# Optimization experiments

Hardware: AMD Instinct MI355X
Metric: run time of the kernel (lower is better)

The kernel has to match this reference:

```python
import jax, jax.numpy as jnp
import numpy as np

CURVE = 1.0
TAU = 0.5
N_NODES = 32768
N_EDGES = 65536
IN_CH = 64
OUT_CH = 64
N_HEADS = 8
N_RF = 128
EPS = 1e-7


def _make_projection_matrix(m, d, seed=0):
    # FAVOR+ projection: stacked rows of transposed QR blocks, row-rescaled by chi norms.
    rng = np.random.RandomState(seed)
    blocks = []
    nb_full = m // d
    for _ in range(nb_full):
        q, _ = np.linalg.qr(rng.randn(d, d))
        blocks.append(q.T)
    rem = m - nb_full * d
    if rem > 0:
        q, _ = np.linalg.qr(rng.randn(d, d))
        blocks.append(q.T[:rem])
    final = np.vstack(blocks)  # [m, d]
    mult = np.linalg.norm(rng.randn(m, d), axis=1)
    return (mult[:, None] * final).astype(np.float32)


def _expmap0(u, c):
    # Hyperboloid exp map at origin; time slot of u is ignored.
    sqrtK = 1.0 / jnp.sqrt(c)
    x = u[..., 1:]
    xn = jnp.maximum(jnp.linalg.norm(x, axis=-1, keepdims=True), EPS)
    theta = xn / sqrtK
    return jnp.concatenate([sqrtK * jnp.cosh(theta), sqrtK * jnp.sinh(theta) * x / xn], axis=-1)


def _proj(x, c):
    # Re-project onto hyperboloid: x0 = sqrt(1/c + ||x_space||^2)
    K = 1.0 / c
    y = x[..., 1:]
    t = jnp.sqrt(K + jnp.sum(y * y, axis=-1, keepdims=True))
    return jnp.concatenate([t, y], axis=-1)


def _logmap0(x, c):
    # Hyperboloid log map at origin; output tangent has zero time component.
    sqrtK = 1.0 / jnp.sqrt(c)
    y = x[..., 1:]
    yn = jnp.maximum(jnp.linalg.norm(y, axis=-1, keepdims=True), EPS)
    t = jnp.maximum(x[..., 0:1] / sqrtK, 1.0 + EPS)
    res = sqrtK * jnp.arccosh(t) * y / yn
    return jnp.concatenate([jnp.zeros_like(res[..., :1]), res], axis=-1)


def _softmax_kernel(data, P, tau, c):
    # Performer-style exp kernel with hyperbolic (time-coordinate) prefactor.
    dt = data[..., 0:1]
    ds = data[..., 1:]
    m = 1.0 / jnp.sqrt(jnp.asarray(P.shape[0], jnp.float32))
    wx = jnp.exp(jnp.einsum('bnhd,dm->bnhm', ds, P) / jnp.sqrt(tau))
    front = jnp.exp((c / tau - dt * dt / tau) / 2.0) * m  # [b,n,h,1]
    return wx * front


def setup_inputs() -> dict:
    key = jax.random.key(0)
    k1, k2, k3, k4 = jax.random.split(key, 4)
    std = (2.0 / (IN_CH + OUT_CH)) ** 0.5
    z = 0.01 * jax.random.normal(k1, (1, N_NODES, IN_CH), jnp.float32)
    Wq = std * jax.random.normal(k2, (N_HEADS, OUT_CH, IN_CH), jnp.float32)
    Wk = std * jax.random.normal(k3, (N_HEADS, OUT_CH, IN_CH), jnp.float32)
    Wv = std * jax.random.normal(k4, (N_HEADS, OUT_CH, IN_CH), jnp.float32)
    edge_index = jax.random.randint(jax.random.fold_in(key, 7), (2, N_EDGES), 0, N_NODES, jnp.int32)
    proj_mat = jnp.asarray(_make_projection_matrix(IN_CH - 1, N_RF))  # [63, 128]
    return {"z": z, "Wq": Wq, "Wk": Wk, "Wv": Wv, "proj_mat": proj_mat, "edge_index": edge_index}


def reference(z, Wq, Wk, Wv, proj_mat, edge_index):
    c = jnp.float32(CURVE)
    tau = jnp.float32(TAU)
    zs = z[0]  # [N, C] (B == 1, squeeze)
    zh = _proj(_expmap0(zs, c), c)  # lift features to hyperboloid
    u = _logmap0(zh, c)             # [N, C], tangent at origin

    def hyplin(W):  # HypLinear (no bias): proj(expmap0(logmap0(x) @ W^T)) for all heads
        mu = jnp.einsum('nc,hoc->hno', u, W)  # [H, N, D]
        return _proj(_expmap0(mu, c), c)

    q, k, v = hyplin(Wq), hyplin(Wk), hyplin(Wv)  # [H, N, D]
    H, N, D = q.shape
    # mirrors torch stacked.reshape(-1, N, H, D) (row-major relabeling)
    query = q.reshape(1, N, H, D)
    key_ = k.reshape(1, N, H, D)
    value = v.reshape(1, N, H, D)

    qp = _softmax_kernel(query, proj_mat, tau, c).transpose(2, 0, 1, 3)  # [H,1,N,M]
    kp = _softmax_kernel(key_, proj_mat, tau, c).transpose(2, 0, 1, 3)   # [H,1,N,M]
    vv = value.transpose(2, 0, 1, 3)                                      # [H,1,N,D]

    last = jnp.einsum('hbnm,hbnd->hbmd', kp, vv)   # [H,1,M,D] kv summary
    zo = jnp.einsum('hbnm,hbmd->hbnd', qp, last)   # [H,1,N,D]
    mnorm = -zo[..., 0:1] ** 2 + jnp.sum(zo[..., 1:] ** 2, axis=-1, keepdims=True)
    zo = zo / (jnp.sqrt(c) * jnp.sqrt(jnp.abs(mnorm)))  # renormalize onto hyperboloid

    start, end = edge_index[0], edge_index[1]
    ea = jnp.einsum('hbem,hbem->hbe', qp[:, :, end, :], kp[:, :, start, :])
    A_weight = ea.transpose(1, 2, 0)  # [1, E, H]

    # hyper_agg: Euclidean head-mean followed by Minkowski renormalization
    t = jnp.mean(zo[:, 0], axis=0)  # [N, D]
    xn = -t[..., 0:1] ** 2 + jnp.sum(t[..., 1:] ** 2, axis=-1, keepdims=True)
    z_next = t / (jnp.sqrt(c) * jnp.sqrt(jnp.abs(xn)))
    link_loss = jnp.mean(A_weight)
    return z_next, link_loss
```

## Files before the change

### kernel.cpp

```cpp
#include <hip/hip_runtime.h>

#define DEV __device__ __forceinline__

#define NNODES 32768
#define NEDGES 65536
#define NROWS  262144
#define EPSF   1e-7f
#define SQRT2F 1.4142135623730951f
#define LOG2E  1.4426950408889634f
#define LOG2SQRT63 2.9886399611087573f

#define OFF_WFRAG 0u
#define OFF_LASTB 0u
#define OFF_PFRAG 196608u
#define OFF_EA    212992u
#define OFF_U     409600u
#define OFF_PART  42352640u
#define OFF_PHIQ  75907072u
#define OFF_PHIK  143015936u

typedef short s8v __attribute__((ext_vector_type(8)));
typedef float f4v __attribute__((ext_vector_type(4)));
typedef float f2v __attribute__((ext_vector_type(2)));

DEV unsigned short f2bf(float f) {
  unsigned u = __float_as_uint(f);
  return (unsigned short)((u + 0x7fffu + ((u >> 16) & 1u)) >> 16);
}
DEV float bf2f(unsigned short h) { return __uint_as_float(((unsigned)h) << 16); }
DEV unsigned pack2(float lo, float hi) {
  return __builtin_amdgcn_perm(__float_as_uint(hi) + 0x8000u, __float_as_uint(lo) + 0x8000u, 0x07060302u);
}
DEV float frcp(float x) { return __builtin_amdgcn_rcpf(x); }
DEV float fsqrt(float x) { return __builtin_amdgcn_sqrtf(x); }
DEV float fexp2(float x) { return __builtin_amdgcn_exp2f(x); }

__global__ __launch_bounds__(256) void k01_prep(const float* __restrict__ z, unsigned short* __restrict__ ubf,
                                                const float* __restrict__ Wq, const float* __restrict__ Wk,
                                                const float* __restrict__ Wv, const float* __restrict__ P,
                                                unsigned short* __restrict__ Wfrag, unsigned short* __restrict__ Pfrag,
                                                float* __restrict__ ea) {
  int i = blockIdx.x * 256 + threadIdx.x;
  float4 v = *(const float4*)(z + (size_t)i * 4);
  if ((i & 15) == 0) v.x = 0.f;
  uint2 pk;
  pk.x = pack2(v.x, v.y);
  pk.y = pack2(v.z, v.w);
  *(uint2*)(ubf + (size_t)i * 4) = pk;

  if (blockIdx.x < 96) {
    if (i == 0) ea[0] = 0.f;
    int stride = 96 * 256;
    for (int t = i; t < 98304; t += stride) {
      int j = t & 7, lane = (t >> 3) & 63, nt = (t >> 9) & 3, ks = (t >> 11) & 1, h = (t >> 12) & 7, sm = t >> 15;
      int k = ks * 32 + (lane >> 4) * 8 + j;
      int n = nt * 16 + (lane & 15);
      const float* W = (sm == 0) ? Wq : ((sm == 1) ? Wk : Wv);
      Wfrag[t] = f2bf(W[(h * 64 + n) * 64 + k]);
    }
    for (int t = i; t < 8192; t += stride) {
      int j = t & 7, lane = (t >> 3) & 63, ks = (t >> 9) & 1, mt = (t >> 10) & 7;
      int k = ks * 32 + (lane >> 4) * 8 + j;
      int r = lane & 15;
      int m = ((mt >> 2) << 6) + ((r >> 2) << 4) + ((mt & 3) << 2) + (r & 3);
      Pfrag[t] = (k == 0) ? (unsigned short)0 : f2bf(P[(k - 1) * 128 + m] * (SQRT2F * LOG2E));
    }
  }
}

__global__ __launch_bounds__(256, 4) void k2_mfma(const unsigned short* __restrict__ ubf,
                                                  const unsigned short* __restrict__ Wfrag,
                                                  const unsigned short* __restrict__ Pfrag,
                                                  unsigned char* __restrict__ phiq, unsigned char* __restrict__ phik,
                                                  unsigned char* __restrict__ part8) {
  __shared__ short lds_raw[9472];
  short* sbuf = lds_raw;
  float* sfront = (float*)(lds_raw + 9216);
  unsigned char* kbufT8 = (unsigned char*)lds_raw;
  unsigned char* vbufT8 = (unsigned char*)lds_raw + 9216;

  int w = threadIdx.x >> 6, lane = threadIdx.x & 63;
  int q = lane >> 4, l = lane & 15;
  int b = blockIdx.x;
  int h = b >> 8, t = b & 255;
  int n0 = t * 128 + w * 32;

  s8v afr[2][2];
#pragma unroll
  for (int mt = 0; mt < 2; ++mt)
#pragma unroll
    for (int ks = 0; ks < 2; ++ks)
      afr[mt][ks] = *(const s8v*)(ubf + (size_t)(n0 + mt * 16 + l) * 64 + ks * 32 + q * 8);

  const s8v* Wf = (const s8v*)Wfrag;
  const s8v* Pf = (const s8v*)Pfrag;
  unsigned vk[2][4];
  unsigned keepA[8], keepB[8];

#pragma unroll
  for (int sm = 0; sm < 3; ++sm) {
    f4v acc[2][4];
#pragma unroll
    for (int mt = 0; mt < 2; ++mt)
#pragma unroll
      for (int nt = 0; nt < 4; ++nt) acc[mt][nt] = (f4v)(0.f);
#pragma unroll
    for (int ks = 0; ks < 2; ++ks)
#pragma unroll
      for (int nt = 0; nt < 4; ++nt) {
        s8v bf = Wf[(((sm * 8 + h) * 2 + ks) * 4 + nt) * 64 + lane];
#pragma unroll
        for (int mt = 0; mt < 2; ++mt)
          acc[mt][nt] = __builtin_amdgcn_mfma_f32_16x16x32_bf16(afr[mt][ks], bf, acc[mt][nt], 0, 0, 0);
      }
#pragma unroll
    for (int mt = 0; mt < 2; ++mt) {
      float rs[4];
#pragma unroll
      for (int reg = 0; reg < 4; ++reg) {
        float v0 = (l == 0) ? 0.f : acc[mt][0][reg];
        rs[reg] = v0 * v0 + acc[mt][1][reg] * acc[mt][1][reg] + acc[mt][2][reg] * acc[mt][2][reg] +
                  acc[mt][3][reg] * acc[mt][3][reg];
      }
#pragma unroll
      for (int reg = 0; reg < 4; ++reg) {
#pragma unroll
        for (int off = 1; off < 16; off <<= 1) rs[reg] += __shfl_xor(rs[reg], off, 64);
      }
      float vreg[4][4];
#pragma unroll
      for (int reg = 0; reg < 4; ++reg) {
        float x = fmaxf(fsqrt(rs[reg]), EPSF);
        float e = fexp2(x * LOG2E);
        float sh = 0.5f * (e - frcp(e));
        float ratio = sh * frcp(x);
        float sh2 = sh * sh;
        int row = mt * 16 + q * 4 + reg;
        if (sm == 2) {
          float tt2 = fsqrt(1.f + sh2);
#pragma unroll
          for (int nt = 0; nt < 4; ++nt) {
            float val = acc[mt][nt][reg] * ratio;
            if (l == 0 && nt == 0) val = tt2;
            vreg[nt][reg] = val;
          }
        } else {
          float lf = -sh2 * LOG2E - LOG2SQRT63;
          if (l == 0) sfront[w * 32 + row] = lf;
#pragma unroll
          for (int nt = 0; nt < 4; ++nt) {
            float val = acc[mt][nt][reg] * ratio;
            if (l == 0 && nt == 0) val = 0.f;
            sbuf[w * 2304 + row * 72 + ((nt * 16 + l) ^ ((q >> 1) << 4))] =
                (short)(__float_as_uint(val) >> 16);
          }
        }
      }
      if (sm == 2) {
#pragma unroll
        for (int nt = 0; nt < 4; ++nt) {
          unsigned pv = __builtin_amdgcn_cvt_pk_fp8_f32(vreg[nt][0], vreg[nt][1], 0, 0);
          vk[mt][nt] = __builtin_amdgcn_cvt_pk_fp8_f32(vreg[nt][2], vreg[nt][3], pv, 1);
        }
      }
    }

    if (sm < 2) {
      int fr = (l >> 3) & 1;
      s8v bsf[2][2];
#pragma unroll
      for (int nt = 0; nt < 2; ++nt)
#pragma unroll
        for (int ks = 0; ks < 2; ++ks)
          bsf[nt][ks] = *(const s8v*)&sbuf[w * 2304 + (nt * 16 + l) * 72 + ((ks * 32 + q * 8) ^ (fr << 4))];
      float lf0 = sfront[w * 32 + l];
      float lf1 = sfront[w * 32 + 16 + l];
      unsigned char* dst = sm ? phik : phiq;
      unsigned g0a[4], g0b[4], g1a[4], g1b[4];
#pragma unroll
      for (int mt = 0; mt < 8; ++mt) {
        f4v a0 = (f4v)(0.f), a1 = (f4v)(0.f);
#pragma unroll
        for (int ks = 0; ks < 2; ++ks) {
          s8v ap = Pf[(mt * 2 + ks) * 64 + lane];
          a0 = __builtin_amdgcn_mfma_f32_16x16x32_bf16(ap, bsf[0][ks], a0, 0, 0, 0);
          a1 = __builtin_amdgcn_mfma_f32_16x16x32_bf16(ap, bsf[1][ks], a1, 0, 0, 0);
        }
        float v00 = fexp2(a0[0] + lf0), v01 = fexp2(a0[1] + lf0), v02 = fexp2(a0[2] + lf0), v03 = fexp2(a0[3] + lf0);
        float v10 = fexp2(a1[0] + lf1), v11 = fexp2(a1[1] + lf1), v12 = fexp2(a1[2] + lf1), v13 = fexp2(a1[3] + lf1);
        unsigned p0 = __builtin_amdgcn_cvt_pk_fp8_f32(v00, v01, 0, 0);
        p0 = __builtin_amdgcn_cvt_pk_fp8_f32(v02, v03, p0, 1);
        unsigned p1 = __builtin_amdgcn_cvt_pk_fp8_f32(v10, v11, 0, 0);
        p1 = __builtin_amdgcn_cvt_pk_fp8_f32(v12, v13, p1, 1);
        if (mt < 4) { g0a[mt] = p0; g1a[mt] = p1; }
        else        { g0b[mt - 4] = p0; g1b[mt - 4] = p1; }
        if (sm == 1) { keepA[mt] = p0; keepB[mt] = p1; }
      }
      size_t b0 = (size_t)(n0 + l) * 1024 + (size_t)(h * 128 + q * 16);
      *(uint4*)(dst + b0)              = make_uint4(g0a[0], g0a[1], g0a[2], g0a[3]);
      *(uint4*)(dst + b0 + 64)         = make_uint4(g0b[0], g0b[1], g0b[2], g0b[3]);
      *(uint4*)(dst + b0 + 16384)      = make_uint4(g1a[0], g1a[1], g1a[2], g1a[3]);
      *(uint4*)(dst + b0 + 16384 + 64) = make_uint4(g1b[0], g1b[1], g1b[2], g1b[3]);
    }
  }

  f4v facc[2][4];
#pragma unroll
  for (int mtl = 0; mtl < 2; ++mtl)
#pragma unroll
    for (int nt = 0; nt < 4; ++nt) facc[mtl][nt] = (f4v)(0.f);

#pragma unroll
  for (int hf = 0; hf < 2; ++hf) {
    __syncthreads();
    if ((w >> 1) == hf) {
      int nd0 = (w & 1) * 32 + l, nd1 = nd0 + 16;
      int c0 = nd0 ^ (q << 4), c1 = nd1 ^ (q << 4);
#pragma unroll
      for (int mt = 0; mt < 8; ++mt) {
        int M0 = ((mt >> 2) << 6) + (q << 4) + ((mt & 3) << 2);
        unsigned a = keepA[mt], bq = keepB[mt];
#pragma unroll
        for (int r = 0; r < 4; ++r) {
          kbufT8[(M0 + r) * 72 + c0] = (unsigned char)(a >> (8 * r));
          kbufT8[(M0 + r) * 72 + c1] = (unsigned char)(bq >> (8 * r));
        }
      }
#pragma unroll
      for (int mt = 0; mt < 2; ++mt)
#pragma unroll
        for (int nt = 0; nt < 4; ++nt)
          *(unsigned*)&vbufT8[(nt * 16 + l) * 72 + (w & 1) * 32 + mt * 16 + q * 4] = vk[mt][nt];
    }
    __syncthreads();
#pragma unroll
    for (int kc = 0; kc < 2; ++kc) {
      long bv[4];
#pragma unroll
      for (int nt = 0; nt < 4; ++nt)
        bv[nt] = *(const long*)&vbufT8[(nt * 16 + l) * 72 + kc * 32 + q * 8];
      long av[2];
#pragma unroll
      for (int mtl = 0; mtl < 2; ++mtl) {
        int row = (2 * w + mtl) * 16 + l;
        int cb = (kc * 32 + q * 8) ^ (((2 * w + mtl) & 3) << 4);
        av[mtl] = *(const long*)&kbufT8[row * 72 + cb];
      }
#pragma unroll
      for (int mtl = 0; mtl < 2; ++mtl)
#pragma unroll
        for (int nt = 0; nt < 4; ++nt)
          facc[mtl][nt] = __builtin_amdgcn_mfma_f32_16x16x32_fp8_fp8(av[mtl], bv[nt], facc[mtl][nt], 0, 0, 0);
    }
  }

#pragma unroll
  for (int mtl = 0; mtl < 2; ++mtl)
#pragma unroll
    for (int nt = 0; nt < 4; ++nt) {
      unsigned pk8 = __builtin_amdgcn_cvt_pk_bf8_f32(facc[mtl][nt][0], facc[mtl][nt][1], 0, 0);
      pk8 = __builtin_amdgcn_cvt_pk_bf8_f32(facc[mtl][nt][2], facc[mtl][nt][3], pk8, 1);
      int d = nt * 16 + l;
      int m = (2 * w + mtl) * 16 + q * 4;
      *(unsigned*)(part8 + ((size_t)((t * 8 + h) * 64 + d)) * 128 + m) = pk8;
    }
}

__global__ __launch_bounds__(256) void k35(const unsigned* __restrict__ part32, unsigned char* __restrict__ lastB,
                                           const unsigned char* __restrict__ phiq,
                                           const unsigned char* __restrict__ phik,
                                           const int* __restrict__ ei, float* __restrict__ ea) {
  int b = blockIdx.x;
  if (b < 64) {
    int t2 = b * 256 + threadIdx.x;
    float s0 = 0.f, s1 = 0.f, s2 = 0.f, s3 = 0.f;
#pragma unroll 8
    for (int c = 0; c < 256; ++c) {
      unsigned v = part32[(c << 14) + t2];
      f2v lo = __builtin_amdgcn_cvt_pk_f32_bf8(v, 0);
      f2v hi = __builtin_amdgcn_cvt_pk_f32_bf8(v, 1);
      s0 += lo.x; s1 += lo.y; s2 += hi.x; s3 += hi.y;
    }
    int mq = t2 & 31, d = (t2 >> 5) & 63, h = t2 >> 11;
    int m0 = mq * 4;
    int ks = m0 >> 5, j0 = m0 & 7, qq = (m0 >> 3) & 3;
    int lane = qq * 16 + (d & 15), nt = d >> 4;
    unsigned r = __builtin_amdgcn_cvt_pk_bf8_f32(s0, s1, 0, 0);
    r = __builtin_amdgcn_cvt_pk_bf8_f32(s2, s3, r, 1);
    *(unsigned*)(lastB + ((((h * 4 + ks) * 4 + nt) * 64 + lane) << 3) + j0) = r;
    return;
  }
  __shared__ float part[4];
  int lane = threadIdx.x & 63, w = threadIdx.x >> 6;
  int wid = (b - 64) * 4 + w;
  float acc0 = 0.f, acc1 = 0.f;
#pragma unroll
  for (int i = 0; i < 8; i += 2) {
    int e0 = wid * 8 + i, e1 = e0 + 1;
    int s0 = ei[e0], d0 = ei[NEDGES + e0];
    int s1 = ei[e1], d1 = ei[NEDGES + e1];
    uint4 qa = *(const uint4*)(phiq + (size_t)d0 * 1024 + lane * 16);
    uint4 ka = *(const uint4*)(phik + (size_t)s0 * 1024 + lane * 16);
    uint4 qb = *(const uint4*)(phiq + (size_t)d1 * 1024 + lane * 16);
    uint4 kb = *(const uint4*)(phik + (size_t)s1 * 1024 + lane * 16);
    unsigned qs[8] = {qa.x, qa.y, qa.z, qa.w, qb.x, qb.y, qb.z, qb.w};
    unsigned ks[8] = {ka.x, ka.y, ka.z, ka.w, kb.x, kb.y, kb.z, kb.w};
#pragma unroll
    for (int p = 0; p < 8; ++p) {
      f2v q0 = __builtin_amdgcn_cvt_pk_f32_fp8(qs[p], 0);
      f2v q1 = __builtin_amdgcn_cvt_pk_f32_fp8(qs[p], 1);
      f2v k0 = __builtin_amdgcn_cvt_pk_f32_fp8(ks[p], 0);
      f2v k1 = __builtin_amdgcn_cvt_pk_f32_fp8(ks[p], 1);
      float t0 = fmaf(q0.x, k0.x, q0.y * k0.y);
      float t1 = fmaf(q1.x, k1.x, q1.y * k1.y);
      if (p < 4) acc0 += t0 + t1; else acc1 += t0 + t1;
    }
  }
  float acc = acc0 + acc1;
#pragma unroll
  for (int o = 1; o < 64; o <<= 1) acc += __shfl_xor(acc, o, 64);
  if (lane == 0) part[w] = acc;
  __syncthreads();
  if (threadIdx.x == 0) atomicAdd(ea, part[0] + part[1] + part[2] + part[3]);
}

__global__ __launch_bounds__(512) void k4_mfma(const unsigned char* __restrict__ phiq,
                                               const unsigned char* __restrict__ lastB,
                                               const float* __restrict__ ea, float* __restrict__ out) {
  __shared__ unsigned zbufT[8][64][18];
  int w = threadIdx.x >> 6, lane = threadIdx.x & 63;
  int q = lane >> 4, l = lane & 15;
  int n0 = blockIdx.x * 32;

  const long* Bf = (const long*)lastB;
  long bf[4][4];
#pragma unroll
  for (int ks = 0; ks < 4; ++ks)
#pragma unroll
    for (int nt = 0; nt < 4; ++nt) bf[ks][nt] = Bf[((w * 4 + ks) * 4 + nt) * 64 + lane];

  long af[2][4];
#pragma unroll
  for (int mt = 0; mt < 2; ++mt)
#pragma unroll
    for (int ks = 0; ks < 4; ++ks)
      af[mt][ks] = *(const long*)(phiq + (size_t)(8 * (n0 + mt * 16 + l) + w) * 128 + ks * 32 + q * 8);

  f4v acc[2][4];
#pragma unroll
  for (int mt = 0; mt < 2; ++mt)
#pragma unroll
    for (int nt = 0; nt < 4; ++nt) acc[mt][nt] = (f4v)(0.f);
#pragma unroll
  for (int ks = 0; ks < 4; ++ks)
#pragma unroll
    for (int nt = 0; nt < 4; ++nt)
#pragma unroll
      for (int mt = 0; mt < 2; ++mt)
        acc[mt][nt] = __builtin_amdgcn_mfma_f32_16x16x32_fp8_bf8(af[mt][ks], bf[ks][nt], acc[mt][nt], 0, 0, 0);

#pragma unroll
  for (int mt = 0; mt < 2; ++mt) {
    float rs[4];
#pragma unroll
    for (int reg = 0; reg < 4; ++reg) {
      float v0 = acc[mt][0][reg];
      float s0 = (l == 0) ? -v0 * v0 : v0 * v0;
      rs[reg] = s0 + acc[mt][1][reg] * acc[mt][1][reg] + acc[mt][2][reg] * acc[mt][2][reg] +
                acc[mt][3][reg] * acc[mt][3][reg];
    }
#pragma unroll
    for (int reg = 0; reg < 4; ++reg) {
#pragma unroll
      for (int off = 1; off < 16; off <<= 1) rs[reg] += __shfl_xor(rs[reg], off, 64);
    }
    float inv[4];
#pragma unroll
    for (int reg = 0; reg < 4; ++reg) inv[reg] = frcp(fsqrt(fabsf(rs[reg])));
#pragma unroll
    for (int nt = 0; nt < 4; ++nt) {
      uint2 pk;
      pk.x = pack2(acc[mt][nt][0] * inv[0], acc[mt][nt][1] * inv[1]);
      pk.y = pack2(acc[mt][nt][2] * inv[2], acc[mt][nt][3] * inv[3]);
      *(uint2*)&zbufT[w][nt * 16 + l][mt * 8 + q * 2] = pk;
    }
  }
  __syncthreads();

  int tid = threadIdx.x;
  int i = tid >> 4, dg = tid & 15;
  int i2 = i >> 1, sel = i & 1;
  float s[4] = {0.f, 0.f, 0.f, 0.f};
#pragma unroll
  for (int w2 = 0; w2 < 8; ++w2) {
#pragma unroll
    for (int j = 0; j < 4; ++j) {
      unsigned u = zbufT[w2][dg * 4 + j][i2];
      s[j] += bf2f((unsigned short)(sel ? (u >> 16) : (u & 0xffffu)));
    }
  }
  float m2 = 0.f;
#pragma unroll
  for (int j = 0; j < 4; ++j) {
    s[j] *= 0.125f;
    m2 += ((dg == 0 && j == 0) ? -s[j] * s[j] : s[j] * s[j]);
  }
#pragma unroll
  for (int off = 1; off < 16; off <<= 1) m2 += __shfl_xor(m2, off, 64);
  float inv = frcp(fsqrt(fabsf(m2)));
  float4 o = make_float4(s[0] * inv, s[1] * inv, s[2] * inv, s[3] * inv);
  *(float4*)(out + (size_t)(n0 + i) * 64 + dg * 4) = o;
  if (blockIdx.x == 0 && tid == 0) out[(size_t)NNODES * 64] = ea[0] * (1.0f / 524288.0f);
}

extern "C" void kernel_launch(void* const* d_in, const int* in_sizes, int n_in,
                              void* d_out, int out_size, void* d_ws, size_t ws_size,
                              hipStream_t stream) {
  const float* z  = (const float*)d_in[0];
  const float* Wq = (const float*)d_in[1];
  const float* Wk = (const float*)d_in[2];
  const float* Wv = (const float*)d_in[3];
  const float* P  = (const float*)d_in[4];
  const int* ei   = (const int*)d_in[5];
  char* ws = (char*)d_ws;
  unsigned short* Wfrag = (unsigned short*)(ws + OFF_WFRAG);
  unsigned char*  lastB = (unsigned char*)(ws + OFF_LASTB);
  unsigned short* Pfrag = (unsigned short*)(ws + OFF_PFRAG);
  float*          ea    = (float*)(ws + OFF_EA);
  unsigned short* ubf   = (unsigned short*)(ws + OFF_U);
  unsigned char*  part8 = (unsigned char*)(ws + OFF_PART);
  unsigned char*  phiq  = (unsigned char*)(ws + OFF_PHIQ);
  unsigned char*  phik  = (unsigned char*)(ws + OFF_PHIK);

  k01_prep<<<2048, 256, 0, stream>>>(z, ubf, Wq, Wk, Wv, P, Wfrag, Pfrag, ea);
  k2_mfma<<<2048, 256, 0, stream>>>(ubf, Wfrag, Pfrag, phiq, phik, part8);
  k35<<<64 + 2048, 256, 0, stream>>>((const unsigned*)part8, lastB, phiq, phik, ei, ea);
  k4_mfma<<<NNODES / 32, 512, 0, stream>>>(phiq, lastB, ea, (float*)d_out);
}
```

Baseline: 178.0 us.

## Stage full K/V fp8 tile in LDS directly and raise k2 occupancy

K and V fp8 fragments are now written straight into a larger LDS tile as they are produced, instead of being held in registers and staged in two halves with extra barriers. The KV-summary MFMA loop then runs once over all 128 rows after a single sync, and launch bounds go from 4 to 5 blocks per CU. The aim is to free the keepA/keepB/vk registers and cut barrier count so occupancy can rise. The cost is more LDS per block, which could limit residency, and byte-granular LDS stores now sit inside the phi computation loop.

```diff
diff --git a/kernel.cpp b/kernel.cpp
--- a/kernel.cpp
+++ b/kernel.cpp
@@ -68,16 +68,16 @@
   }
 }
 
-__global__ __launch_bounds__(256, 4) void k2_mfma(const unsigned short* __restrict__ ubf,
+__global__ __launch_bounds__(256, 5) void k2_mfma(const unsigned short* __restrict__ ubf,
                                                   const unsigned short* __restrict__ Wfrag,
                                                   const unsigned short* __restrict__ Pfrag,
                                                   unsigned char* __restrict__ phiq, unsigned char* __restrict__ phik,
                                                   unsigned char* __restrict__ part8) {
-  __shared__ short lds_raw[9472];
+  __shared__ short lds_raw[13312];
   short* sbuf = lds_raw;
-  float* sfront = (float*)(lds_raw + 9216);
-  unsigned char* kbufT8 = (unsigned char*)lds_raw;
-  unsigned char* vbufT8 = (unsigned char*)lds_raw + 9216;
+  float* sfront = (float*)(lds_raw + 13056);
+  unsigned char* kbuf2 = (unsigned char*)lds_raw;
+  unsigned char* vbuf2 = (unsigned char*)lds_raw + 17408;
 
   int w = threadIdx.x >> 6, lane = threadIdx.x & 63;
   int q = lane >> 4, l = lane & 15;
@@ -94,8 +94,6 @@
 
   const s8v* Wf = (const s8v*)Wfrag;
   const s8v* Pf = (const s8v*)Pfrag;
-  unsigned vk[2][4];
-  unsigned keepA[8], keepB[8];
 
 #pragma unroll
   for (int sm = 0; sm < 3; ++sm) {
@@ -160,7 +158,8 @@
 #pragma unroll
         for (int nt = 0; nt < 4; ++nt) {
           unsigned pv = __builtin_amdgcn_cvt_pk_fp8_f32(vreg[nt][0], vreg[nt][1], 0, 0);
-          vk[mt][nt] = __builtin_amdgcn_cvt_pk_fp8_f32(vreg[nt][2], vreg[nt][3], pv, 1);
+          pv = __builtin_amdgcn_cvt_pk_fp8_f32(vreg[nt][2], vreg[nt][3], pv, 1);
+          *(unsigned*)&vbuf2[(nt * 16 + l) * 136 + w * 32 + mt * 16 + q * 4] = pv;
         }
       }
     }
@@ -175,8 +174,10 @@
           bsf[nt][ks] = *(const s8v*)&sbuf[w * 2304 + (nt * 16 + l) * 72 + ((ks * 32 + q * 8) ^ (fr << 4))];
       float lf0 = sfront[w * 32 + l];
       float lf1 = sfront[w * 32 + 16 + l];
+      if (sm == 1) __syncthreads();
       unsigned char* dst = sm ? phik : phiq;
       unsigned g0a[4], g0b[4], g1a[4], g1b[4];
+      int c0 = (w * 32 + l) ^ (q << 4), c1 = (w * 32 + 16 + l) ^ (q << 4);
 #pragma unroll
       for (int mt = 0; mt < 8; ++mt) {
         f4v a0 = (f4v)(0.f), a1 = (f4v)(0.f);
@@ -194,7 +195,14 @@
         p1 = __builtin_amdgcn_cvt_pk_fp8_f32(v12, v13, p1, 1);
         if (mt < 4) { g0a[mt] = p0; g1a[mt] = p1; }
         else        { g0b[mt - 4] = p0; g1b[mt - 4] = p1; }
-        if (sm == 1) { keepA[mt] = p0; keepB[mt] = p1; }
+        if (sm == 1) {
+          int M0 = ((mt >> 2) << 6) + (q << 4) + ((mt & 3) << 2);
+#pragma unroll
+          for (int r = 0; r < 4; ++r) {
+            kbuf2[(M0 + r) * 136 + c0] = (unsigned char)(p0 >> (8 * r));
+            kbuf2[(M0 + r) * 136 + c1] = (unsigned char)(p1 >> (8 * r));
+          }
+        }
       }
       size_t b0 = (size_t)(n0 + l) * 1024 + (size_t)(h * 128 + q * 16);
       *(uint4*)(dst + b0)              = make_uint4(g0a[0], g0a[1], g0a[2], g0a[3]);
@@ -204,6 +212,7 @@
     }
   }
 
+  __syncthreads();
   f4v facc[2][4];
 #pragma unroll
   for (int mtl = 0; mtl < 2; ++mtl)
@@ -211,47 +220,23 @@
     for (int nt = 0; nt < 4; ++nt) facc[mtl][nt] = (f4v)(0.f);
 
 #pragma unroll
-  for (int hf = 0; hf < 2; ++hf) {
-    __syncthreads();
-    if ((w >> 1) == hf) {
-      int nd0 = (w & 1) * 32 + l, nd1 = nd0 + 16;
-      int c0 = nd0 ^ (q << 4), c1 = nd1 ^ (q << 4);
-#pragma unroll
-      for (int mt = 0; mt < 8; ++mt) {
-        int M0 = ((mt >> 2) << 6) + (q << 4) + ((mt & 3) << 2);
-        unsigned a = keepA[mt], bq = keepB[mt];
-#pragma unroll
-        for (int r = 0; r < 4; ++r) {
-          kbufT8[(M0 + r) * 72 + c0] = (unsigned char)(a >> (8 * r));
-          kbufT8[(M0 + r) * 72 + c1] = (unsigned char)(bq >> (8 * r));
-        }
-      }
-#pragma unroll
-      for (int mt = 0; mt < 2; ++mt)
-#pragma unroll
-        for (int nt = 0; nt < 4; ++nt)
-          *(unsigned*)&vbufT8[(nt * 16 + l) * 72 + (w & 1) * 32 + mt * 16 + q * 4] = vk[mt][nt];
-    }
-    __syncthreads();
-#pragma unroll
-    for (int kc = 0; kc < 2; ++kc) {
-      long bv[4];
+  for (int kc = 0; kc < 4; ++kc) {
+    long bv[4];
+#pragma unroll
+    for (int nt = 0; nt < 4; ++nt)
+      bv[nt] = *(const long*)&vbuf2[(nt * 16 + l) * 136 + kc * 32 + q * 8];
+    long av[2];
+#pragma unroll
+    for (int mtl = 0; mtl < 2; ++mtl) {
+      int row = (2 * w + mtl) * 16 + l;
+      int cb = (kc * 32 + q * 8) ^ (((2 * w + mtl) & 3) << 4);
+      av[mtl] = *(const long*)&kbuf2[row * 136 + cb];
+    }
+#pragma unroll
+    for (int mtl = 0; mtl < 2; ++mtl)
 #pragma unroll
       for (int nt = 0; nt < 4; ++nt)
-        bv[nt] = *(const long*)&vbufT8[(nt * 16 + l) * 72 + kc * 32 + q * 8];
-      long av[2];
-#pragma unroll
-      for (int mtl = 0; mtl < 2; ++mtl) {
-        int row = (2 * w + mtl) * 16 + l;
-        int cb = (kc * 32 + q * 8) ^ (((2 * w + mtl) & 3) << 4);
-        av[mtl] = *(const long*)&kbufT8[row * 72 + cb];
-      }
-#pragma unroll
-      for (int mtl = 0; mtl < 2; ++mtl)
-#pragma unroll
-        for (int nt = 0; nt < 4; ++nt)
-          facc[mtl][nt] = __builtin_amdgcn_mfma_f32_16x16x32_fp8_fp8(av[mtl], bv[nt], facc[mtl][nt], 0, 0, 0);
-    }
+        facc[mtl][nt] = __builtin_amdgcn_mfma_f32_16x16x32_fp8_fp8(av[mtl], bv[nt], facc[mtl][nt], 0, 0, 0);
   }
 
 #pragma unroll
```

New measurement: 187.1 us. +5.1%, slower.

## Move edge-score reduction into final kernel and parallelize partial-sum reduction

Applied to the files above, without the earlier changes.

The edge attention dot-product work moves out of the reduction kernel and into the final output kernel, interleaved as odd blocks alongside the output blocks. A completion counter with atomics lets the last finishing block write the link loss. The lastB reduction kernel now splits the 256-chunk sum across four lane groups and combines them with shuffles, using 256 blocks instead of 64. This aims to shorten the serial reduction stage and overlap the gather-heavy edge work with the final MFMA compute, at the cost of an extra atomic counter and fence logic.

```diff
diff --git a/kernel.cpp b/kernel.cpp
--- a/kernel.cpp
+++ b/kernel.cpp
@@ -49,7 +49,7 @@
   *(uint2*)(ubf + (size_t)i * 4) = pk;
 
   if (blockIdx.x < 96) {
-    if (i == 0) ea[0] = 0.f;
+    if (i == 0) { ea[0] = 0.f; ((unsigned*)ea)[1] = 0u; }
     int stride = 96 * 256;
     for (int t = i; t < 98304; t += stride) {
       int j = t & 7, lane = (t >> 3) & 63, nt = (t >> 9) & 3, ks = (t >> 11) & 1, h = (t >> 12) & 7, sm = t >> 15;
@@ -266,71 +266,89 @@
     }
 }
 
-__global__ __launch_bounds__(256) void k35(const unsigned* __restrict__ part32, unsigned char* __restrict__ lastB,
-                                           const unsigned char* __restrict__ phiq,
-                                           const unsigned char* __restrict__ phik,
-                                           const int* __restrict__ ei, float* __restrict__ ea) {
-  int b = blockIdx.x;
-  if (b < 64) {
-    int t2 = b * 256 + threadIdx.x;
-    float s0 = 0.f, s1 = 0.f, s2 = 0.f, s3 = 0.f;
-#pragma unroll 8
-    for (int c = 0; c < 256; ++c) {
-      unsigned v = part32[(c << 14) + t2];
-      f2v lo = __builtin_amdgcn_cvt_pk_f32_bf8(v, 0);
-      f2v hi = __builtin_amdgcn_cvt_pk_f32_bf8(v, 1);
-      s0 += lo.x; s1 += lo.y; s2 += hi.x; s3 += hi.y;
-    }
+__global__ __launch_bounds__(256) void k35(const unsigned* __restrict__ part32, unsigned char* __restrict__ lastB) {
+  int lane = threadIdx.x & 63, w2 = threadIdx.x >> 6;
+  int r = lane & 15, cg = lane >> 4;
+  int t2 = blockIdx.x * 64 + w2 * 16 + r;
+  float s0 = 0.f, s1 = 0.f, s2 = 0.f, s3 = 0.f;
+  int cbase = cg * 64;
+#pragma unroll 16
+  for (int ci = 0; ci < 64; ++ci) {
+    unsigned v = part32[((cbase + ci) << 14) + t2];
+    f2v lo = __builtin_amdgcn_cvt_pk_f32_bf8(v, 0);
+    f2v hi = __builtin_amdgcn_cvt_pk_f32_bf8(v, 1);
+    s0 += lo.x; s1 += lo.y; s2 += hi.x; s3 += hi.y;
+  }
+  s0 += __shfl_xor(s0, 16, 64); s1 += __shfl_xor(s1, 16, 64);
+  s2 += __shfl_xor(s2, 16, 64); s3 += __shfl_xor(s3, 16, 64);
+  s0 += __shfl_xor(s0, 32, 64); s1 += __shfl_xor(s1, 32, 64);
+  s2 += __shfl_xor(s2, 32, 64); s3 += __shfl_xor(s3, 32, 64);
+  if (lane < 16) {
     int mq = t2 & 31, d = (t2 >> 5) & 63, h = t2 >> 11;
     int m0 = mq * 4;
     int ks = m0 >> 5, j0 = m0 & 7, qq = (m0 >> 3) & 3;
-    int lane = qq * 16 + (d & 15), nt = d >> 4;
-    unsigned r = __builtin_amdgcn_cvt_pk_bf8_f32(s0, s1, 0, 0);
-    r = __builtin_amdgcn_cvt_pk_bf8_f32(s2, s3, r, 1);
-    *(unsigned*)(lastB + ((((h * 4 + ks) * 4 + nt) * 64 + lane) << 3) + j0) = r;
-    return;
-  }
-  __shared__ float part[4];
-  int lane = threadIdx.x & 63, w = threadIdx.x >> 6;
-  int wid = (b - 64) * 4 + w;
-  float acc0 = 0.f, acc1 = 0.f;
-#pragma unroll
-  for (int i = 0; i < 8; i += 2) {
-    int e0 = wid * 8 + i, e1 = e0 + 1;
-    int s0 = ei[e0], d0 = ei[NEDGES + e0];
-    int s1 = ei[e1], d1 = ei[NEDGES + e1];
-    uint4 qa = *(const uint4*)(phiq + (size_t)d0 * 1024 + lane * 16);
-    uint4 ka = *(const uint4*)(phik + (size_t)s0 * 1024 + lane * 16);
-    uint4 qb = *(const uint4*)(phiq + (size_t)d1 * 1024 + lane * 16);
-    uint4 kb = *(const uint4*)(phik + (size_t)s1 * 1024 + lane * 16);
-    unsigned qs[8] = {qa.x, qa.y, qa.z, qa.w, qb.x, qb.y, qb.z, qb.w};
-    unsigned ks[8] = {ka.x, ka.y, ka.z, ka.w, kb.x, kb.y, kb.z, kb.w};
-#pragma unroll
-    for (int p = 0; p < 8; ++p) {
-      f2v q0 = __builtin_amdgcn_cvt_pk_f32_fp8(qs[p], 0);
-      f2v q1 = __builtin_amdgcn_cvt_pk_f32_fp8(qs[p], 1);
-      f2v k0 = __builtin_amdgcn_cvt_pk_f32_fp8(ks[p], 0);
-      f2v k1 = __builtin_amdgcn_cvt_pk_f32_fp8(ks[p], 1);
-      float t0 = fmaf(q0.x, k0.x, q0.y * k0.y);
-      float t1 = fmaf(q1.x, k1.x, q1.y * k1.y);
-      if (p < 4) acc0 += t0 + t1; else acc1 += t0 + t1;
-    }
-  }
-  float acc = acc0 + acc1;
-#pragma unroll
-  for (int o = 1; o < 64; o <<= 1) acc += __shfl_xor(acc, o, 64);
-  if (lane == 0) part[w] = acc;
-  __syncthreads();
-  if (threadIdx.x == 0) atomicAdd(ea, part[0] + part[1] + part[2] + part[3]);
+    int ln = qq * 16 + (d & 15), nt = d >> 4;
+    unsigned rr = __builtin_amdgcn_cvt_pk_bf8_f32(s0, s1, 0, 0);
+    rr = __builtin_amdgcn_cvt_pk_bf8_f32(s2, s3, rr, 1);
+    *(unsigned*)(lastB + ((((h * 4 + ks) * 4 + nt) * 64 + ln) << 3) + j0) = rr;
+  }
 }
 
 __global__ __launch_bounds__(512) void k4_mfma(const unsigned char* __restrict__ phiq,
+                                               const unsigned char* __restrict__ phik,
                                                const unsigned char* __restrict__ lastB,
-                                               const float* __restrict__ ea, float* __restrict__ out) {
+                                               const int* __restrict__ ei,
+                                               float* __restrict__ ea, float* __restrict__ out) {
   __shared__ unsigned zbufT[8][64][18];
   int w = threadIdx.x >> 6, lane = threadIdx.x & 63;
+
+  if (blockIdx.x & 1) {
+    float* part = (float*)zbufT;
+    int wid = (blockIdx.x >> 1) * 8 + w;
+    float acc0 = 0.f, acc1 = 0.f;
+#pragma unroll
+    for (int i = 0; i < 8; i += 2) {
+      int e0 = wid * 8 + i, e1 = e0 + 1;
+      int s0 = ei[e0], d0 = ei[NEDGES + e0];
+      int s1 = ei[e1], d1 = ei[NEDGES + e1];
+      uint4 qa = *(const uint4*)(phiq + (size_t)d0 * 1024 + lane * 16);
+      uint4 ka = *(const uint4*)(phik + (size_t)s0 * 1024 + lane * 16);
+      uint4 qb = *(const uint4*)(phiq + (size_t)d1 * 1024 + lane * 16);
+      uint4 kb = *(const uint4*)(phik + (size_t)s1 * 1024 + lane * 16);
+      unsigned qs[8] = {qa.x, qa.y, qa.z, qa.w, qb.x, qb.y, qb.z, qb.w};
+      unsigned ks[8] = {ka.x, ka.y, ka.z, ka.w, kb.x, kb.y, kb.z, kb.w};
+#pragma unroll
+      for (int p = 0; p < 8; ++p) {
+        f2v q0 = __builtin_amdgcn_cvt_pk_f32_fp8(qs[p], 0);
+        f2v q1 = __builtin_amdgcn_cvt_pk_f32_fp8(qs[p], 1);
+        f2v k0 = __builtin_amdgcn_cvt_pk_f32_fp8(ks[p], 0);
+        f2v k1 = __builtin_amdgcn_cvt_pk_f32_fp8(ks[p], 1);
+        float t0 = fmaf(q0.x, k0.x, q0.y * k0.y);
+        float t1 = fmaf(q1.x, k1.x, q1.y * k1.y);
+        if (p < 4) acc0 += t0 + t1; else acc1 += t0 + t1;
+      }
+    }
+    float acc = acc0 + acc1;
+#pragma unroll
+    for (int o = 1; o < 64; o <<= 1) acc += __shfl_xor(acc, o, 64);
+    if (lane == 0) part[w] = acc;
+    __syncthreads();
+    if (threadIdx.x == 0) {
+      float tot = part[0] + part[1] + part[2] + part[3] + part[4] + part[5] + part[6] + part[7];
+      atomicAdd(ea, tot);
+      __threadfence();
+      unsigned old = atomicAdd((unsigned*)ea + 1, 1u);
+      if (old == 1023u) {
+        __threadfence();
+        float fin = atomicAdd(ea, 0.f);
+        out[(size_t)NNODES * 64] = fin * (1.0f / 524288.0f);
+      }
+    }
+    return;
+  }
+
   int q = lane >> 4, l = lane & 15;
-  int n0 = blockIdx.x * 32;
+  int n0 = (blockIdx.x >> 1) * 32;
 
   const long* Bf = (const long*)lastB;
   long bf[4][4];
@@ -410,7 +428,6 @@
   float inv = frcp(fsqrt(fabsf(m2)));
   float4 o = make_float4(s[0] * inv, s[1] * inv, s[2] * inv, s[3] * inv);
   *(float4*)(out + (size_t)(n0 + i) * 64 + dg * 4) = o;
-  if (blockIdx.x == 0 && tid == 0) out[(size_t)NNODES * 64] = ea[0] * (1.0f / 524288.0f);
 }
 
 extern "C" void kernel_launch(void* const* d_in, const int* in_sizes, int n_in,
@@ -434,6 +451,6 @@
 
   k01_prep<<<2048, 256, 0, stream>>>(z, ubf, Wq, Wk, Wv, P, Wfrag, Pfrag, ea);
   k2_mfma<<<2048, 256, 0, stream>>>(ubf, Wfrag, Pfrag, phiq, phik, part8);
-  k35<<<64 + 2048, 256, 0, stream>>>((const unsigned*)part8, lastB, phiq, phik, ei, ea);
-  k4_mfma<<<NNODES / 32, 512, 0, stream>>>(phiq, lastB, ea, (float*)d_out);
-}
+  k35<<<256, 256, 0, stream>>>((const unsigned*)part8, lastB);
+  k4_mfma<<<2048, 512, 0, stream>>>(phiq, phik, lastB, ei, ea, (float*)d_out);
+}
```

Result: slower. 226.0 us (+26.9%).
